# Kernel optimization log

Measured on AMD Instinct MI355X. Metric: run time of the kernel, lower is better.

The kernel has to match this reference:

```python
import jax, jax.numpy as jnp
import numpy as np

B, S, IN_DIM, OUT_DIM = 8, 8192, 1024, 1024


def setup_inputs() -> dict:
    key = jax.random.key(0)
    k1, k2, k3, k4 = jax.random.split(key, 4)
    x = jax.random.normal(k1, (B, S, IN_DIM), dtype=jnp.float32)
    visual_mask = jax.random.randint(k2, (B, S), 0, 2) == 1  # bool [B,S]
    # nn.Linear weights are [out_dim, in_dim]
    w_v = jax.random.normal(k3, (OUT_DIM, IN_DIM), dtype=jnp.float32) * (IN_DIM ** -0.5)
    w_t = jax.random.normal(k4, (OUT_DIM, IN_DIM), dtype=jnp.float32) * (IN_DIM ** -0.5)
    return {"x": x, "visual_mask": visual_mask, "w_v": w_v, "w_t": w_t}


def reference(x, visual_mask, w_v, w_t):
    # Per-token routed dual linear: out[b,s] = x[b,s] @ (w_v if mask else w_t).T
    out_v = jnp.einsum("bsi,oi->bso", x, w_v)  # [B,S,OUT]
    out_t = jnp.einsum("bsi,oi->bso", x, w_t)  # [B,S,OUT]
    return jnp.where(visual_mask[:, :, None], out_v, out_t)
```

## Files before the change

kernel.cpp:

```cpp
#include <hip/hip_runtime.h>
#include <stdint.h>

#define TOKENS 65536
#define KDIM 1024
#define NDIM 1024
#define MROWS 65664
#define ROWTILES 513
#define BK 64

using short8 = __attribute__((ext_vector_type(8))) short;
using f32x4  = __attribute__((ext_vector_type(4))) float;

#define ASYNC_COPY16(g, l) __builtin_amdgcn_global_load_lds( \
    (const __attribute__((address_space(1))) void*)(g),      \
    (__attribute__((address_space(3))) void*)(l), 16, 0, 0)

__device__ __forceinline__ short f2bf(float f) {
    union { float f; unsigned u; } c; c.f = f;
    unsigned r = c.u + 0x7FFFu + ((c.u >> 16) & 1u);
    return (short)(r >> 16);
}

__global__ __launch_bounds__(256) void detect_mask_fmt(const unsigned* __restrict__ mask,
                                                       int* __restrict__ hdr) {
    int i = blockIdx.x * 256 + threadIdx.x;
    unsigned w = mask[i];
    int mode = 0;
    if (w == 0x3F800000u)      mode = 2;
    else if (w > 1u)           mode = 1;
    if (mode) atomicMax(&hdr[2], mode);
}

__device__ __forceinline__ bool read_mask(const void* mask, int fmt, int t) {
    if (fmt == 2) return ((const float*)mask)[t] != 0.0f;
    if (fmt == 1) return ((const unsigned char*)mask)[t] != 0;
    return ((const int*)mask)[t] != 0;
}

__global__ __launch_bounds__(256) void route_assign(const void* __restrict__ mask,
                                                    int* __restrict__ rowmap,
                                                    int* __restrict__ slotmap,
                                                    int* __restrict__ hdr) {
    const int tid  = threadIdx.x;
    const int lane = tid & 63;
    const int wid  = tid >> 6;
    const int t    = blockIdx.x * 256 + tid;
    const int fmt  = hdr[2];
    const bool m   = read_mask(mask, fmt, t);

    unsigned long long bal = __ballot(m);
    int vpre = __popcll(bal & ((1ull << lane) - 1ull));
    int vcnt = __popcll(bal);
    int tpre = lane - vpre;
    int tcnt = 64 - vcnt;

    __shared__ int cv[4], ct[4], ov[4], ot[4];
    __shared__ int bv, bt;
    if (lane == 0) { cv[wid] = vcnt; ct[wid] = tcnt; }
    __syncthreads();
    if (tid == 0) {
        int sv = 0, st = 0;
        for (int w = 0; w < 4; ++w) { ov[w] = sv; sv += cv[w]; ot[w] = st; st += ct[w]; }
        bv = atomicAdd(&hdr[0], sv);
        bt = atomicAdd(&hdr[1], st);
    }
    __syncthreads();
    int slot = m ? (bv + ov[wid] + vpre)
                 : (MROWS - 1 - (bt + ot[wid] + tpre));
    rowmap[slot] = t;
    slotmap[t] = slot;
}

__global__ __launch_bounds__(256) void gather_convert(const float* __restrict__ x,
                                                      const int* __restrict__ slotmap,
                                                      short* __restrict__ Abuf) {
    const int lane = threadIdx.x & 63;
    const int t    = blockIdx.x * 4 + (threadIdx.x >> 6);
    const int slot = slotmap[t];
    const float* src = x + (size_t)t * KDIM;
    short* dst = Abuf + (size_t)slot * KDIM;
#pragma unroll
    for (int p = 0; p < 4; ++p) {
        int k = p * 256 + lane * 4;
        float4 v = *(const float4*)(src + k);
        short4 o;
        o.x = f2bf(v.x); o.y = f2bf(v.y); o.z = f2bf(v.z); o.w = f2bf(v.w);
        *(short4*)(dst + k) = o;
    }
}

__global__ __launch_bounds__(256) void convert_weights(const float* __restrict__ wv,
                                                       const float* __restrict__ wt,
                                                       short* __restrict__ ovp,
                                                       short* __restrict__ otp) {
    int i = (blockIdx.x * 256 + threadIdx.x) * 4;
    const float* src; short* dst; int off;
    if (i < NDIM * KDIM) { src = wv; dst = ovp; off = i; }
    else                 { src = wt; dst = otp; off = i - NDIM * KDIM; }
    float4 v = *(const float4*)(src + off);
    short4 o;
    o.x = f2bf(v.x); o.y = f2bf(v.y); o.z = f2bf(v.z); o.w = f2bf(v.w);
    *(short4*)(dst + off) = o;
}

__global__ __launch_bounds__(256) void gemm_routed(const short* __restrict__ Abuf,
                                                   const short* __restrict__ Wv,
                                                   const short* __restrict__ Wt,
                                                   const int* __restrict__ rowmap,
                                                   const int* __restrict__ hdr,
                                                   float* __restrict__ out) {
    __shared__ __align__(16) short As[128 * BK];
    __shared__ __align__(16) short Bs[128 * BK];
    __shared__ int rmap_s[128];

    const int bid = blockIdx.x;
    const int w   = (bid & 7) * ROWTILES + (bid >> 3);
    const int r0  = (w >> 3) * 128;
    const int n0  = (w & 7) * 128;

    const int Mv = hdr[0];
    if (r0 == Mv) return;
    const short* Wsel = (r0 < Mv) ? Wv : Wt;

    const int tid  = threadIdx.x;
    const int lane = tid & 63;
    const int wvid = tid >> 6;

    if (tid < 128) rmap_s[tid] = rowmap[r0 + tid];

    const int srow = wvid * 32 + (lane >> 3);
    const int scol = (lane & 7) * 8;
    const short* aP = Abuf + (size_t)(r0 + srow) * KDIM + scol;
    const short* bP = Wsel + (size_t)(n0 + srow) * KDIM + scol;
    char* lA = (char*)As + wvid * 4096;
    char* lB = (char*)Bs + wvid * 4096;

    f32x4 acc[4][4];
#pragma unroll
    for (int i = 0; i < 4; ++i)
#pragma unroll
        for (int j = 0; j < 4; ++j) acc[i][j] = f32x4{0.f, 0.f, 0.f, 0.f};

    const int wm = (wvid & 1) * 64;
    const int wn = (wvid >> 1) * 64;
    const short* aF = As + (wm + (lane & 15)) * BK + (lane >> 4) * 8;
    const short* bF = Bs + (wn + (lane & 15)) * BK + (lane >> 4) * 8;

    for (int kt = 0; kt < KDIM / BK; ++kt) {
        const int k0 = kt * BK;
        __syncthreads();
#pragma unroll
        for (int c = 0; c < 4; ++c) {
            ASYNC_COPY16(aP + (size_t)c * 8 * KDIM + k0, lA + c * 1024);
            ASYNC_COPY16(bP + (size_t)c * 8 * KDIM + k0, lB + c * 1024);
        }
        __syncthreads();

#pragma unroll
        for (int ks = 0; ks < 2; ++ks) {
            short8 af[4], bfr[4];
#pragma unroll
            for (int mt = 0; mt < 4; ++mt) af[mt]  = *(const short8*)(aF + mt * 16 * BK + ks * 32);
#pragma unroll
            for (int nt = 0; nt < 4; ++nt) bfr[nt] = *(const short8*)(bF + nt * 16 * BK + ks * 32);
#pragma unroll
            for (int mt = 0; mt < 4; ++mt)
#pragma unroll
                for (int nt = 0; nt < 4; ++nt)
                    acc[mt][nt] = __builtin_amdgcn_mfma_f32_16x16x32_bf16(
                        af[mt], bfr[nt], acc[mt][nt], 0, 0, 0);
        }
    }

    const int col = n0 + wn + (lane & 15);
#pragma unroll
    for (int mt = 0; mt < 4; ++mt) {
        int rb = wm + mt * 16 + ((lane >> 4) << 2);
#pragma unroll
        for (int i = 0; i < 4; ++i) {
            int token = rmap_s[rb + i];
            if (token < 0) continue;
            float* orow = out + (size_t)token * NDIM + col;
            orow[0]  = acc[mt][0][i];
            orow[16] = acc[mt][1][i];
            orow[32] = acc[mt][2][i];
            orow[48] = acc[mt][3][i];
        }
    }
}

__global__ __launch_bounds__(256) void fallback_matvec(const float* __restrict__ x,
                                                       const void* __restrict__ mask,
                                                       const float* __restrict__ wv,
                                                       const float* __restrict__ wt,
                                                       const int* __restrict__ hdr,
                                                       float* __restrict__ out) {
    __shared__ float xs[KDIM];
    const int t = blockIdx.x;
    const int fmt = hdr[2];
    const bool m = read_mask(mask, fmt, t);
    const float* w = m ? wv : wt;
    const float* src = x + (size_t)t * KDIM;
    for (int k = threadIdx.x; k < KDIM; k += 256) xs[k] = src[k];
    __syncthreads();
    for (int n = threadIdx.x; n < NDIM; n += 256) {
        const float* wr = w + (size_t)n * KDIM;
        float s = 0.f;
        for (int k = 0; k < KDIM; ++k) s += xs[k] * wr[k];
        out[(size_t)t * NDIM + n] = s;
    }
}

extern "C" void kernel_launch(void* const* d_in, const int* in_sizes, int n_in,
                              void* d_out, int out_size, void* d_ws, size_t ws_size,
                              hipStream_t stream) {
    const float* x    = (const float*)d_in[0];
    const void*  mask = d_in[1];
    const float* w_v  = (const float*)d_in[2];
    const float* w_t  = (const float*)d_in[3];
    float* out = (float*)d_out;

    char* ws = (char*)d_ws;
    int*   hdr     = (int*)ws;
    int*   rowmap  = (int*)(ws + 4096);
    int*   slotmap = (int*)(ws + 270336);
    short* wvb     = (short*)(ws + 532480);
    short* wtb     = (short*)(ws + 2629632);
    short* Abuf    = (short*)(ws + 4726784);
    const size_t need = 4726784ull + (size_t)MROWS * KDIM * sizeof(short);

    if (ws_size >= need) {
        hipMemsetAsync(hdr, 0, 16, stream);
        hipMemsetAsync(rowmap, 0xFF, MROWS * sizeof(int), stream);
        detect_mask_fmt<<<64, 256, 0, stream>>>((const unsigned*)mask, hdr);
        route_assign<<<TOKENS / 256, 256, 0, stream>>>(mask, rowmap, slotmap, hdr);
        gather_convert<<<TOKENS / 4, 256, 0, stream>>>(x, slotmap, Abuf);
        convert_weights<<<(2 * NDIM * KDIM) / (256 * 4), 256, 0, stream>>>(w_v, w_t, wvb, wtb);
        gemm_routed<<<8 * ROWTILES, 256, 0, stream>>>(Abuf, wvb, wtb, rowmap, hdr, out);
    } else {
        hipMemsetAsync(hdr, 0, 16, stream);
        detect_mask_fmt<<<64, 256, 0, stream>>>((const unsigned*)mask, hdr);
        fallback_matvec<<<TOKENS, 256, 0, stream>>>(x, mask, w_v, w_t, hdr, out);
    }
}
```

Before: 709.5 us.

## Rewrite routed GEMM with 256x256 tiles, double-buffered LDS and swizzled layout

Replaces the 128x128 single-buffered GEMM with a 256x256 tile, 512-thread kernel. It double-buffers the LDS K-tiles, interleaves the async global-to-LDS copies between MFMA quads, and separates phases with explicit barriers, waitcnts and setprio. It also adds an XOR swizzle against LDS bank conflicts and remaps workgroups per XCD. Row tiles go to 256, so routed padding grows, and the large accumulator array raises register pressure.

```diff
diff --git a/kernel.cpp b/kernel.cpp
--- a/kernel.cpp
+++ b/kernel.cpp
@@ -4,9 +4,12 @@
 #define TOKENS 65536
 #define KDIM 1024
 #define NDIM 1024
-#define MROWS 65664
-#define ROWTILES 513
+#define MROWS 65792
+#define ROWTILES 257
+#define NTILES 4
+#define NWG (ROWTILES * NTILES)
 #define BK 64
+#define NT 16
 
 using short8 = __attribute__((ext_vector_type(8))) short;
 using f32x4  = __attribute__((ext_vector_type(4))) float;
@@ -103,20 +106,107 @@
     *(short4*)(dst + off) = o;
 }
 
-__global__ __launch_bounds__(256) void gemm_routed(const short* __restrict__ Abuf,
-                                                   const short* __restrict__ Wv,
-                                                   const short* __restrict__ Wt,
-                                                   const int* __restrict__ rowmap,
-                                                   const int* __restrict__ hdr,
-                                                   float* __restrict__ out) {
-    __shared__ __align__(16) short As[128 * BK];
-    __shared__ __align__(16) short Bs[128 * BK];
-    __shared__ int rmap_s[128];
-
-    const int bid = blockIdx.x;
-    const int w   = (bid & 7) * ROWTILES + (bid >> 3);
-    const int r0  = (w >> 3) * 128;
-    const int n0  = (w & 7) * 128;
+
+#define QUAD(MB, NB)                                                              \
+    do {                                                                          \
+        _Pragma("unroll") for (int m_ = 0; m_ < 4; ++m_)                          \
+        _Pragma("unroll") for (int n_ = 0; n_ < 2; ++n_)                          \
+        _Pragma("unroll") for (int ks_ = 0; ks_ < 2; ++ks_)                       \
+            acc[(MB) + m_][(NB) + n_] = __builtin_amdgcn_mfma_f32_16x16x32_bf16(  \
+                a[2 * m_ + ks_], b[2 * ((NB) + n_) + ks_],                        \
+                acc[(MB) + m_][(NB) + n_], 0, 0, 0);                              \
+    } while (0)
+
+template<bool STAGE, int ENDM>
+__device__ __forceinline__ void kstep(const char* pA, const char* pB,
+                                      char* lA, char* lB,
+                                      const short* aS, const short* bS,
+                                      f32x4 (&acc)[8][4], int xorhi) {
+    short8 a[8], b[8];
+#pragma unroll
+    for (int m = 0; m < 4; ++m) {
+        a[2*m]   = *(const short8*)(pA + m * 2048 + (0  ^ xorhi));
+        a[2*m+1] = *(const short8*)(pA + m * 2048 + (64 ^ xorhi));
+    }
+#pragma unroll
+    for (int n = 0; n < 4; ++n) {
+        b[2*n]   = *(const short8*)(pB + n * 2048 + (0  ^ xorhi));
+        b[2*n+1] = *(const short8*)(pB + n * 2048 + (64 ^ xorhi));
+    }
+    __builtin_amdgcn_s_barrier();
+    asm volatile("s_waitcnt lgkmcnt(0)" ::: "memory");
+    __builtin_amdgcn_sched_barrier(0);
+    __builtin_amdgcn_s_setprio(1);
+    QUAD(0, 0);
+    __builtin_amdgcn_s_setprio(0);
+    __builtin_amdgcn_s_barrier();
+    if (STAGE) {
+        ASYNC_COPY16(bS,                     lB);
+        ASYNC_COPY16(bS + (size_t)64 * KDIM, lB + 8192);
+    }
+    __builtin_amdgcn_s_barrier();
+    __builtin_amdgcn_s_setprio(1);
+    QUAD(0, 2);
+    __builtin_amdgcn_s_setprio(0);
+    __builtin_amdgcn_s_barrier();
+#pragma unroll
+    for (int m = 0; m < 4; ++m) {
+        a[2*m]   = *(const short8*)(pA + (4 + m) * 2048 + (0  ^ xorhi));
+        a[2*m+1] = *(const short8*)(pA + (4 + m) * 2048 + (64 ^ xorhi));
+    }
+    if (STAGE) {
+        ASYNC_COPY16(bS + (size_t)128 * KDIM, lB + 16384);
+        ASYNC_COPY16(bS + (size_t)192 * KDIM, lB + 16384 + 8192);
+    }
+    __builtin_amdgcn_s_barrier();
+    asm volatile("s_waitcnt lgkmcnt(0)" ::: "memory");
+    __builtin_amdgcn_sched_barrier(0);
+    __builtin_amdgcn_s_setprio(1);
+    QUAD(4, 0);
+    __builtin_amdgcn_s_setprio(0);
+    __builtin_amdgcn_s_barrier();
+    if (STAGE) {
+        ASYNC_COPY16(aS,                      lA);
+        ASYNC_COPY16(aS + (size_t)64  * KDIM, lA + 8192);
+        ASYNC_COPY16(aS + (size_t)128 * KDIM, lA + 16384);
+        ASYNC_COPY16(aS + (size_t)192 * KDIM, lA + 16384 + 8192);
+    }
+    __builtin_amdgcn_s_barrier();
+    __builtin_amdgcn_s_setprio(1);
+    QUAD(4, 2);
+    __builtin_amdgcn_s_setprio(0);
+    if (ENDM == 0) asm volatile("s_waitcnt vmcnt(8)" ::: "memory");
+    if (ENDM == 1) asm volatile("s_waitcnt vmcnt(0)" ::: "memory");
+    if (ENDM < 2)  __builtin_amdgcn_s_barrier();
+}
+
+__device__ __forceinline__ void stage_ktile(char* lA, char* lB,
+                                            const short* aS, const short* bS) {
+    ASYNC_COPY16(aS,                      lA);
+    ASYNC_COPY16(aS + (size_t)64  * KDIM, lA + 8192);
+    ASYNC_COPY16(aS + (size_t)128 * KDIM, lA + 16384);
+    ASYNC_COPY16(aS + (size_t)192 * KDIM, lA + 16384 + 8192);
+    ASYNC_COPY16(bS,                      lB);
+    ASYNC_COPY16(bS + (size_t)64  * KDIM, lB + 8192);
+    ASYNC_COPY16(bS + (size_t)128 * KDIM, lB + 16384);
+    ASYNC_COPY16(bS + (size_t)192 * KDIM, lB + 16384 + 8192);
+}
+
+__global__ __launch_bounds__(512, 2) void gemm_routed(const short* __restrict__ Abuf,
+                                                      const short* __restrict__ Wv,
+                                                      const short* __restrict__ Wt,
+                                                      const int* __restrict__ rowmap,
+                                                      const int* __restrict__ hdr,
+                                                      float* __restrict__ out) {
+    __shared__ __align__(16) short As[2 * 256 * 64];
+    __shared__ __align__(16) short Bs[2 * 256 * 64];
+    __shared__ int rmap_s[256];
+
+    const int q = NWG / 8, r = NWG % 8;
+    const int xcd = blockIdx.x & 7, ii = blockIdx.x >> 3;
+    const int wgid = (xcd < r ? xcd * (q + 1) : r * (q + 1) + (xcd - r) * q) + ii;
+    const int r0 = (wgid >> 2) * 256;
+    const int n0 = (wgid & 3) * 256;
 
     const int Mv = hdr[0];
     if (r0 == Mv) return;
@@ -125,66 +215,61 @@
     const int tid  = threadIdx.x;
     const int lane = tid & 63;
     const int wvid = tid >> 6;
-
-    if (tid < 128) rmap_s[tid] = rowmap[r0 + tid];
-
-    const int srow = wvid * 32 + (lane >> 3);
-    const int scol = (lane & 7) * 8;
-    const short* aP = Abuf + (size_t)(r0 + srow) * KDIM + scol;
-    const short* bP = Wsel + (size_t)(n0 + srow) * KDIM + scol;
-    char* lA = (char*)As + wvid * 4096;
-    char* lB = (char*)Bs + wvid * 4096;
-
-    f32x4 acc[4][4];
-#pragma unroll
-    for (int i = 0; i < 4; ++i)
-#pragma unroll
-        for (int j = 0; j < 4; ++j) acc[i][j] = f32x4{0.f, 0.f, 0.f, 0.f};
-
-    const int wm = (wvid & 1) * 64;
-    const int wn = (wvid >> 1) * 64;
-    const short* aF = As + (wm + (lane & 15)) * BK + (lane >> 4) * 8;
-    const short* bF = Bs + (wn + (lane & 15)) * BK + (lane >> 4) * 8;
-
-    for (int kt = 0; kt < KDIM / BK; ++kt) {
-        const int k0 = kt * BK;
-        __syncthreads();
-#pragma unroll
-        for (int c = 0; c < 4; ++c) {
-            ASYNC_COPY16(aP + (size_t)c * 8 * KDIM + k0, lA + c * 1024);
-            ASYNC_COPY16(bP + (size_t)c * 8 * KDIM + k0, lB + c * 1024);
-        }
-        __syncthreads();
-
-#pragma unroll
-        for (int ks = 0; ks < 2; ++ks) {
-            short8 af[4], bfr[4];
-#pragma unroll
-            for (int mt = 0; mt < 4; ++mt) af[mt]  = *(const short8*)(aF + mt * 16 * BK + ks * 32);
-#pragma unroll
-            for (int nt = 0; nt < 4; ++nt) bfr[nt] = *(const short8*)(bF + nt * 16 * BK + ks * 32);
-#pragma unroll
-            for (int mt = 0; mt < 4; ++mt)
-#pragma unroll
-                for (int nt = 0; nt < 4; ++nt)
-                    acc[mt][nt] = __builtin_amdgcn_mfma_f32_16x16x32_bf16(
-                        af[mt], bfr[nt], acc[mt][nt], 0, 0, 0);
-        }
-    }
-
-    const int col = n0 + wn + (lane & 15);
-#pragma unroll
-    for (int mt = 0; mt < 4; ++mt) {
-        int rb = wm + mt * 16 + ((lane >> 4) << 2);
-#pragma unroll
-        for (int i = 0; i < 4; ++i) {
-            int token = rmap_s[rb + i];
+    const int wr   = wvid >> 2;
+    const int wc   = wvid & 3;
+
+    if (tid < 256) rmap_s[tid] = rowmap[r0 + tid];
+
+    const int arow = tid >> 3;
+    const int achk = (tid & 7) ^ (arow & 7);
+    const short* aSrc = Abuf + (size_t)(r0 + arow) * KDIM + achk * 8;
+    const short* bSrc = Wsel + (size_t)(n0 + arow) * KDIM + achk * 8;
+    char* lA0 = (char*)As + wvid * 1024;
+    char* lB0 = (char*)Bs + wvid * 1024;
+    char* lA1 = lA0 + 32768;
+    char* lB1 = lB0 + 32768;
+
+    const int xorhi = (lane & 4) << 4;
+    const char* aRd = (const char*)As + wr * 16384 + (lane & 15) * 128
+                      + (((lane >> 4) * 16) ^ ((lane & 3) << 4));
+    const char* bRd = (const char*)Bs + (wc >> 1) * 16384
+                      + (((wc & 1) * 64 + (lane & 15)) * 128)
+                      + (((lane >> 4) * 16) ^ ((lane & 3) << 4));
+    const char* pA0 = aRd;       const char* pA1 = aRd + 32768;
+    const char* pB0 = bRd;       const char* pB1 = bRd + 32768;
+
+    f32x4 acc[8][4];
+#pragma unroll
+    for (int m = 0; m < 8; ++m)
+#pragma unroll
+        for (int n = 0; n < 4; ++n) acc[m][n] = f32x4{0.f, 0.f, 0.f, 0.f};
+
+    stage_ktile(lA0, lB0, aSrc + 0 * BK, bSrc + 0 * BK);
+    stage_ktile(lA1, lB1, aSrc + 1 * BK, bSrc + 1 * BK);
+    asm volatile("s_waitcnt vmcnt(8)" ::: "memory");
+    __builtin_amdgcn_s_barrier();
+
+    for (int it = 0; it < 7; ++it) {
+        const int k2 = 2 * it + 2, k3 = 2 * it + 3;
+        kstep<true, 0>(pA0, pB0, lA0, lB0, aSrc + k2 * BK, bSrc + k2 * BK, acc, xorhi);
+        kstep<true, 0>(pA1, pB1, lA1, lB1, aSrc + k3 * BK, bSrc + k3 * BK, acc, xorhi);
+    }
+    kstep<false, 1>(pA0, pB0, lA0, lB0, aSrc, bSrc, acc, xorhi);
+    kstep<false, 2>(pA1, pB1, lA1, lB1, aSrc, bSrc, acc, xorhi);
+
+    const int colbase = n0 + wc * 64 + (lane & 15);
+#pragma unroll
+    for (int m = 0; m < 8; ++m) {
+        const int rb = wr * 128 + m * 16 + ((lane >> 4) << 2);
+#pragma unroll
+        for (int i2 = 0; i2 < 4; ++i2) {
+            int token = rmap_s[rb + i2];
             if (token < 0) continue;
-            float* orow = out + (size_t)token * NDIM + col;
-            orow[0]  = acc[mt][0][i];
-            orow[16] = acc[mt][1][i];
-            orow[32] = acc[mt][2][i];
-            orow[48] = acc[mt][3][i];
+            float* orow = out + (size_t)token * NDIM + colbase;
+            orow[0]  = acc[m][0][i2];
+            orow[16] = acc[m][1][i2];
+            orow[32] = acc[m][2][i2];
+            orow[48] = acc[m][3][i2];
         }
     }
 }
@@ -236,7 +321,7 @@
         route_assign<<<TOKENS / 256, 256, 0, stream>>>(mask, rowmap, slotmap, hdr);
         gather_convert<<<TOKENS / 4, 256, 0, stream>>>(x, slotmap, Abuf);
         convert_weights<<<(2 * NDIM * KDIM) / (256 * 4), 256, 0, stream>>>(w_v, w_t, wvb, wtb);
-        gemm_routed<<<8 * ROWTILES, 256, 0, stream>>>(Abuf, wvb, wtb, rowmap, hdr, out);
+        gemm_routed<<<NWG, 512, 0, stream>>>(Abuf, wvb, wtb, rowmap, hdr, out);
     } else {
         hipMemsetAsync(hdr, 0, 16, stream);
         detect_mask_fmt<<<64, 256, 0, stream>>>((const unsigned*)mask, hdr);
```

Result: faster. 653.9 us (-7.8%).
